# Optimization experiments

Measured on AMD Instinct MI355X. Metric: run time of the kernel, lower is better.

## Reference

```python
import jax, jax.numpy as jnp
import numpy as np

NUM_CLASSES = 7


def setup_inputs() -> dict:
    key = jax.random.key(0)
    k1, k2, k3, k4 = jax.random.split(key, 4)
    B, C, D = 65536, NUM_CLASSES, 512
    outputs = jax.random.normal(k1, (B, C), dtype=jnp.float32)
    features = jax.random.normal(k2, (B, D), dtype=jnp.float32)
    targets = jax.random.randint(k3, (B,), 0, C, dtype=jnp.int64)
    attention_weights = jax.random.uniform(k4, (B, D), dtype=jnp.float32)
    return {"outputs": outputs, "features": features, "targets": targets,
            "attention_weights": attention_weights}


def reference(outputs, features, targets, attention_weights):
    lambda_val = 0.1
    B = features.shape[0]
    C = outputs.shape[1]

    # Cross-entropy (mean over batch), matching nn.CrossEntropyLoss
    logp = jax.nn.log_softmax(outputs, axis=-1)  # [B, C]
    ce_loss = -jnp.mean(jnp.take_along_axis(logp, targets[:, None], axis=1))

    # Per-class centers via segment reduce (replaces python loop over classes)
    sums = jax.ops.segment_sum(features, targets, num_segments=C)      # [C, D]
    counts = jax.ops.segment_sum(jnp.ones((B,), features.dtype), targets,
                                 num_segments=C)                        # [C]
    present = counts > 0
    centers = sums / jnp.maximum(counts, 1.0)[:, None]                  # [C, D]

    # Squared distance to own-class center (replaces python loop over batch);
    # samples whose class is absent (impossible here, but kept faithful) add 0.
    diff = features - centers[targets]                                  # [B, D]
    per_sample = jnp.sum(diff * diff, axis=-1) * present[targets].astype(features.dtype)
    center_loss = jnp.sum(per_sample) / B

    l1_loss = jnp.mean(jnp.abs(attention_weights))

    total_loss = ce_loss + lambda_val * center_loss + 0.01 * l1_loss
    return (total_loss, ce_loss, center_loss, l1_loss)
```

## Files before the change

### kernel.cpp

```cpp
#include <hip/hip_runtime.h>

static constexpr int BATCH = 65536;
static constexpr int DDIM  = 512;
static constexpr int NCLS  = 7;
static constexpr int SLICE = NCLS * DDIM;
static constexpr int NSC   = 64;

struct WS {
  double sumsq_s[NSC];
  double l1_s[NSC];
  double ce_s[NSC];
  double wcss;
  double pad;
  float  counts_s[NSC][8];
};
static_assert(sizeof(WS) <= 4096, "header must fit in 4 KB");

__global__ __launch_bounds__(512, 6) void k_main(const float4* __restrict__ F,
                                                 const float4* __restrict__ A,
                                                 const int* __restrict__ tg,
                                                 const float* __restrict__ outputs,
                                                 float* __restrict__ part,
                                                 WS* __restrict__ ws,
                                                 int rpb) {
  const int tid  = threadIdx.x;
  const int bid  = blockIdx.x;
  const int c4   = tid & 127;
  const int ph   = tid >> 7;
  const int slot = bid & (NSC - 1);
  const int base = bid * rpb;

  float4 acc[NCLS];
#pragma unroll
  for (int c = 0; c < NCLS; ++c) acc[c] = make_float4(0.f, 0.f, 0.f, 0.f);
  float sumsq = 0.f, l1 = 0.f;

#pragma unroll 2
  for (int r = base; r < base + rpb; r += 8) {
    const int4 ta = *reinterpret_cast<const int4*>(tg + r);
    const int4 tb = *reinterpret_cast<const int4*>(tg + r + 4);
    const size_t i0 = (size_t)(r + ph) * 128 + c4;
    const float4 f0 = F[i0];
    const float4 f1 = F[i0 + 512];
    const float4 w0 = A[i0];
    const float4 w1 = A[i0 + 512];
    const int t0 = (ph == 0) ? ta.x : (ph == 1) ? ta.y : (ph == 2) ? ta.z : ta.w;
    const int t1 = (ph == 0) ? tb.x : (ph == 1) ? tb.y : (ph == 2) ? tb.z : tb.w;

    sumsq = fmaf(f0.x, f0.x, sumsq); sumsq = fmaf(f0.y, f0.y, sumsq);
    sumsq = fmaf(f0.z, f0.z, sumsq); sumsq = fmaf(f0.w, f0.w, sumsq);
    sumsq = fmaf(f1.x, f1.x, sumsq); sumsq = fmaf(f1.y, f1.y, sumsq);
    sumsq = fmaf(f1.z, f1.z, sumsq); sumsq = fmaf(f1.w, f1.w, sumsq);
    l1 += fabsf(w0.x) + fabsf(w0.y) + fabsf(w0.z) + fabsf(w0.w) +
          fabsf(w1.x) + fabsf(w1.y) + fabsf(w1.z) + fabsf(w1.w);

#pragma unroll
    for (int c = 0; c < NCLS; ++c) {
      acc[c].x += (t0 == c) ? f0.x : 0.f;
      acc[c].y += (t0 == c) ? f0.y : 0.f;
      acc[c].z += (t0 == c) ? f0.z : 0.f;
      acc[c].w += (t0 == c) ? f0.w : 0.f;
      acc[c].x += (t1 == c) ? f1.x : 0.f;
      acc[c].y += (t1 == c) ? f1.y : 0.f;
      acc[c].z += (t1 == c) ? f1.z : 0.f;
      acc[c].w += (t1 == c) ? f1.w : 0.f;
    }
  }

  __shared__ float red[256][33];
  if (ph >= 2) {
    float* row = red[(ph - 2) * 128 + c4];
#pragma unroll
    for (int c = 0; c < NCLS; ++c) {
      row[c * 4 + 0] = acc[c].x; row[c * 4 + 1] = acc[c].y;
      row[c * 4 + 2] = acc[c].z; row[c * 4 + 3] = acc[c].w;
    }
    row[28] = sumsq; row[29] = l1;
  }
  __syncthreads();
  if (ph < 2) {
    const float* row = red[ph * 128 + c4];
#pragma unroll
    for (int c = 0; c < NCLS; ++c) {
      acc[c].x += row[c * 4 + 0]; acc[c].y += row[c * 4 + 1];
      acc[c].z += row[c * 4 + 2]; acc[c].w += row[c * 4 + 3];
    }
    sumsq += row[28]; l1 += row[29];
  }
  __syncthreads();
  if (ph == 1) {
    float* row = red[c4];
#pragma unroll
    for (int c = 0; c < NCLS; ++c) {
      row[c * 4 + 0] = acc[c].x; row[c * 4 + 1] = acc[c].y;
      row[c * 4 + 2] = acc[c].z; row[c * 4 + 3] = acc[c].w;
    }
    row[28] = sumsq; row[29] = l1;
  }
  __syncthreads();

  __shared__ float s2[2], s3[2];
  if (ph == 0) {
    const float* row = red[c4];
#pragma unroll
    for (int c = 0; c < NCLS; ++c) {
      acc[c].x += row[c * 4 + 0]; acc[c].y += row[c * 4 + 1];
      acc[c].z += row[c * 4 + 2]; acc[c].w += row[c * 4 + 3];
    }
    sumsq += row[28]; l1 += row[29];

    float4* __restrict__ myp = reinterpret_cast<float4*>(part + (size_t)bid * SLICE);
#pragma unroll
    for (int c = 0; c < NCLS; ++c) myp[c * 128 + c4] = acc[c];

    float bs = sumsq, bl = l1;
#pragma unroll
    for (int off = 32; off > 0; off >>= 1) {
      bs += __shfl_down(bs, off);
      bl += __shfl_down(bl, off);
    }
    if ((tid & 63) == 0) { s2[tid >> 6] = bs; s3[tid >> 6] = bl; }
  }
  __syncthreads();
  if (tid == 0) {
    atomicAdd(&ws->sumsq_s[slot], (double)(s2[0] + s2[1]));
    atomicAdd(&ws->l1_s[slot],    (double)(s3[0] + s3[1]));
  }

  const int lane = tid & 63, wid = tid >> 6;
  if (wid * 64 < rpb) {
    float ce = 0.f;
    float cw[NCLS];
#pragma unroll
    for (int c = 0; c < NCLS; ++c) cw[c] = 0.f;
    for (int r0 = wid * 64; r0 < rpb; r0 += 512) {
      const int r = r0 + lane;
      const bool ok = (r < rpb);
      const int row = base + (ok ? r : 0);
      const float* o = outputs + (size_t)row * NCLS;
      const float x0 = o[0], x1 = o[1], x2 = o[2], x3 = o[3],
                  x4 = o[4], x5 = o[5], x6 = o[6];
      const float m = fmaxf(fmaxf(fmaxf(x0, x1), fmaxf(x2, x3)),
                            fmaxf(fmaxf(x4, x5), x6));
      const float s = expf(x0 - m) + expf(x1 - m) + expf(x2 - m) + expf(x3 - m) +
                      expf(x4 - m) + expf(x5 - m) + expf(x6 - m);
      const int t = ok ? tg[row] : -1;
      const float xt = (t == 0) ? x0 : (t == 1) ? x1 : (t == 2) ? x2 :
                       (t == 3) ? x3 : (t == 4) ? x4 : (t == 5) ? x5 : x6;
      ce += ok ? ((m - xt) + logf(s)) : 0.f;
#pragma unroll
      for (int c = 0; c < NCLS; ++c)
        cw[c] += (float)__popcll(__ballot(t == c)) * ((lane == 0) ? 1.f : 0.f);
    }
#pragma unroll
    for (int off = 32; off > 0; off >>= 1) ce += __shfl_down(ce, off);
    if (lane == 0) {
      atomicAdd(&ws->ce_s[slot], (double)ce);
#pragma unroll
      for (int c = 0; c < NCLS; ++c) atomicAdd(&ws->counts_s[slot][c], cw[c]);
    }
  }
}

__global__ __launch_bounds__(256) void k_reduce(const float* __restrict__ part,
                                                WS* __restrict__ ws, int nblk) {
  const int c  = blockIdx.x >> 4;
  const int cg = blockIdx.x & 15;
  const int t  = threadIdx.x;
  const int col = cg * 32 + (t & 31);
  const int sl0 = t >> 5;

  float s = 0.f;
#pragma unroll 4
  for (int sl = sl0; sl < nblk; sl += 8)
    s += part[(size_t)sl * SLICE + c * DDIM + col];

  __shared__ float red[8][33];
  red[sl0][t & 31] = s;

  __shared__ float scnt;
  if (t < 64) {
    float cv = ws->counts_s[t][c];
#pragma unroll
    for (int off = 32; off > 0; off >>= 1) cv += __shfl_down(cv, off);
    if (t == 0) scnt = cv;
  }
  __syncthreads();

  if (t < 32) {
    float S = 0.f;
#pragma unroll
    for (int i = 0; i < 8; ++i) S += red[i][t];
    float q = S * S;
#pragma unroll
    for (int off = 16; off > 0; off >>= 1) q += __shfl_down(q, off);
    if (t == 0 && scnt > 0.f) atomicAdd(&ws->wcss, (double)(q / scnt));
  }
}

__global__ __launch_bounds__(64) void k_fin(const WS* __restrict__ ws,
                                            float* __restrict__ out) {
  const int t = threadIdx.x;
  double a = ws->sumsq_s[t], b = ws->l1_s[t], d = ws->ce_s[t];
#pragma unroll
  for (int off = 32; off > 0; off >>= 1) {
    a += __shfl_down(a, off);
    b += __shfl_down(b, off);
    d += __shfl_down(d, off);
  }
  if (t == 0) {
    const double center = (a - ws->wcss) / (double)BATCH;
    const double ce = d / (double)BATCH;
    const double l1 = b / ((double)BATCH * (double)DDIM);
    out[0] = (float)(ce + 0.1 * center + 0.01 * l1);
    out[1] = (float)ce;
    out[2] = (float)center;
    out[3] = (float)l1;
  }
}

extern "C" void kernel_launch(void* const* d_in, const int* in_sizes, int n_in,
                              void* d_out, int out_size, void* d_ws, size_t ws_size,
                              hipStream_t stream) {
  const float*  outputs  = (const float*)d_in[0];
  const float4* features = (const float4*)d_in[1];
  const int*    targets  = (const int*)d_in[2];
  const float4* aw       = (const float4*)d_in[3];
  float* out = (float*)d_out;
  WS* ws = (WS*)d_ws;
  float* part = (float*)((char*)d_ws + 4096);

  const size_t avail = (ws_size > 4096) ? ws_size - 4096 : 0;
  int nblk = 128;
  if (avail >= (size_t)1024 * SLICE * 4) nblk = 1024;
  else if (avail >= (size_t)512 * SLICE * 4) nblk = 512;
  else if (avail >= (size_t)256 * SLICE * 4) nblk = 256;
  const int rpb = BATCH / nblk;

  hipMemsetAsync(d_ws, 0, 4096, stream);

  k_main<<<nblk, 512, 0, stream>>>(features, aw, targets, outputs, part, ws, rpb);
  k_reduce<<<NCLS * 16, 256, 0, stream>>>(part, ws, nblk);
  k_fin<<<1, 64, 0, stream>>>(ws, out);
}
```

Before: 70.75 us.

## Replace global atomics and memset with per-block scalar partials; template rows-per-block

Drops the workspace memset and the double-precision global atomics for sumsq, l1, ce and class counts. Each block now writes its scalar partials next to its per-class feature sums, and a wider final kernel reduces them. Rows-per-block becomes a template parameter so bounds checks vanish. The maximum grid is capped at 512 blocks instead of 1024, which may lower parallelism in the main streaming kernel.

```diff
diff --git a/kernel.cpp b/kernel.cpp
--- a/kernel.cpp
+++ b/kernel.cpp
@@ -1,34 +1,23 @@
 #include <hip/hip_runtime.h>
 
-static constexpr int BATCH = 65536;
-static constexpr int DDIM  = 512;
-static constexpr int NCLS  = 7;
-static constexpr int SLICE = NCLS * DDIM;
-static constexpr int NSC   = 64;
-
-struct WS {
-  double sumsq_s[NSC];
-  double l1_s[NSC];
-  double ce_s[NSC];
-  double wcss;
-  double pad;
-  float  counts_s[NSC][8];
-};
-static_assert(sizeof(WS) <= 4096, "header must fit in 4 KB");
-
+static constexpr int BATCH  = 65536;
+static constexpr int DDIM   = 512;
+static constexpr int NCLS   = 7;
+static constexpr int SLICE  = NCLS * DDIM;
+static constexpr int SLICEP = SLICE + 16;
+static constexpr int NRED   = NCLS * 16;
+
+template <int RPB>
 __global__ __launch_bounds__(512, 6) void k_main(const float4* __restrict__ F,
                                                  const float4* __restrict__ A,
                                                  const int* __restrict__ tg,
                                                  const float* __restrict__ outputs,
-                                                 float* __restrict__ part,
-                                                 WS* __restrict__ ws,
-                                                 int rpb) {
+                                                 float* __restrict__ part) {
   const int tid  = threadIdx.x;
   const int bid  = blockIdx.x;
   const int c4   = tid & 127;
   const int ph   = tid >> 7;
-  const int slot = bid & (NSC - 1);
-  const int base = bid * rpb;
+  const int base = bid * RPB;
 
   float4 acc[NCLS];
 #pragma unroll
@@ -36,7 +25,7 @@
   float sumsq = 0.f, l1 = 0.f;
 
 #pragma unroll 2
-  for (int r = base; r < base + rpb; r += 8) {
+  for (int r = base; r < base + RPB; r += 8) {
     const int4 ta = *reinterpret_cast<const int4*>(tg + r);
     const int4 tb = *reinterpret_cast<const int4*>(tg + r + 4);
     const size_t i0 = (size_t)(r + ph) * 128 + c4;
@@ -109,7 +98,7 @@
     }
     sumsq += row[28]; l1 += row[29];
 
-    float4* __restrict__ myp = reinterpret_cast<float4*>(part + (size_t)bid * SLICE);
+    float4* __restrict__ myp = reinterpret_cast<float4*>(part + (size_t)bid * SLICEP);
 #pragma unroll
     for (int c = 0; c < NCLS; ++c) myp[c * 128 + c4] = acc[c];
 
@@ -121,22 +110,18 @@
     }
     if ((tid & 63) == 0) { s2[tid >> 6] = bs; s3[tid >> 6] = bl; }
   }
-  __syncthreads();
-  if (tid == 0) {
-    atomicAdd(&ws->sumsq_s[slot], (double)(s2[0] + s2[1]));
-    atomicAdd(&ws->l1_s[slot],    (double)(s3[0] + s3[1]));
-  }
-
+
+  constexpr int NACT = (RPB / 64 < 8) ? RPB / 64 : 8;
+  __shared__ float ce_w[8];
+  __shared__ float cw_w[8][8];
   const int lane = tid & 63, wid = tid >> 6;
-  if (wid * 64 < rpb) {
+  if (wid < NACT) {
     float ce = 0.f;
     float cw[NCLS];
 #pragma unroll
     for (int c = 0; c < NCLS; ++c) cw[c] = 0.f;
-    for (int r0 = wid * 64; r0 < rpb; r0 += 512) {
-      const int r = r0 + lane;
-      const bool ok = (r < rpb);
-      const int row = base + (ok ? r : 0);
+    for (int r0 = wid * 64; r0 < RPB; r0 += NACT * 64) {
+      const int row = base + r0 + lane;
       const float* o = outputs + (size_t)row * NCLS;
       const float x0 = o[0], x1 = o[1], x2 = o[2], x3 = o[3],
                   x4 = o[4], x5 = o[5], x6 = o[6];
@@ -144,10 +129,10 @@
                             fmaxf(fmaxf(x4, x5), x6));
       const float s = expf(x0 - m) + expf(x1 - m) + expf(x2 - m) + expf(x3 - m) +
                       expf(x4 - m) + expf(x5 - m) + expf(x6 - m);
-      const int t = ok ? tg[row] : -1;
+      const int t = tg[row];
       const float xt = (t == 0) ? x0 : (t == 1) ? x1 : (t == 2) ? x2 :
                        (t == 3) ? x3 : (t == 4) ? x4 : (t == 5) ? x5 : x6;
-      ce += ok ? ((m - xt) + logf(s)) : 0.f;
+      ce += (m - xt) + logf(s);
 #pragma unroll
       for (int c = 0; c < NCLS; ++c)
         cw[c] += (float)__popcll(__ballot(t == c)) * ((lane == 0) ? 1.f : 0.f);
@@ -155,15 +140,35 @@
 #pragma unroll
     for (int off = 32; off > 0; off >>= 1) ce += __shfl_down(ce, off);
     if (lane == 0) {
-      atomicAdd(&ws->ce_s[slot], (double)ce);
-#pragma unroll
-      for (int c = 0; c < NCLS; ++c) atomicAdd(&ws->counts_s[slot][c], cw[c]);
-    }
+      ce_w[wid] = ce;
+#pragma unroll
+      for (int c = 0; c < NCLS; ++c) cw_w[wid][c] = cw[c];
+    }
+  }
+  __syncthreads();
+
+  if (tid == 0) {
+    float ceb = 0.f, cb[NCLS];
+#pragma unroll
+    for (int c = 0; c < NCLS; ++c) cb[c] = 0.f;
+#pragma unroll
+    for (int w = 0; w < NACT; ++w) {
+      ceb += ce_w[w];
+#pragma unroll
+      for (int c = 0; c < NCLS; ++c) cb[c] += cw_w[w][c];
+    }
+    float* sp = part + (size_t)bid * SLICEP + SLICE;
+    sp[0] = s2[0] + s2[1];
+    sp[1] = s3[0] + s3[1];
+    sp[2] = ceb;
+#pragma unroll
+    for (int c = 0; c < NCLS; ++c) sp[3 + c] = cb[c];
   }
 }
 
 __global__ __launch_bounds__(256) void k_reduce(const float* __restrict__ part,
-                                                WS* __restrict__ ws, int nblk) {
+                                                double* __restrict__ qpart,
+                                                int nblk) {
   const int c  = blockIdx.x >> 4;
   const int cg = blockIdx.x & 15;
   const int t  = threadIdx.x;
@@ -173,18 +178,10 @@
   float s = 0.f;
 #pragma unroll 4
   for (int sl = sl0; sl < nblk; sl += 8)
-    s += part[(size_t)sl * SLICE + c * DDIM + col];
+    s += part[(size_t)sl * SLICEP + c * DDIM + col];
 
   __shared__ float red[8][33];
   red[sl0][t & 31] = s;
-
-  __shared__ float scnt;
-  if (t < 64) {
-    float cv = ws->counts_s[t][c];
-#pragma unroll
-    for (int off = 32; off > 0; off >>= 1) cv += __shfl_down(cv, off);
-    if (t == 0) scnt = cv;
-  }
   __syncthreads();
 
   if (t < 32) {
@@ -194,28 +191,86 @@
     float q = S * S;
 #pragma unroll
     for (int off = 16; off > 0; off >>= 1) q += __shfl_down(q, off);
-    if (t == 0 && scnt > 0.f) atomicAdd(&ws->wcss, (double)(q / scnt));
+    if (t == 0) qpart[blockIdx.x] = (double)q;
   }
 }
 
-__global__ __launch_bounds__(64) void k_fin(const WS* __restrict__ ws,
-                                            float* __restrict__ out) {
+__global__ __launch_bounds__(512) void k_fin(const float* __restrict__ part,
+                                             const double* __restrict__ qpart,
+                                             float* __restrict__ out, int nblk) {
   const int t = threadIdx.x;
-  double a = ws->sumsq_s[t], b = ws->l1_s[t], d = ws->ce_s[t];
+  const int lane = t & 63, wid = t >> 6;
+
+  double ss = 0.0, l1 = 0.0, ce = 0.0;
+  float cnt[NCLS];
+#pragma unroll
+  for (int c = 0; c < NCLS; ++c) cnt[c] = 0.f;
+  for (int sl = t; sl < nblk; sl += 512) {
+    const float* sp = part + (size_t)sl * SLICEP + SLICE;
+    ss += (double)sp[0];
+    l1 += (double)sp[1];
+    ce += (double)sp[2];
+#pragma unroll
+    for (int c = 0; c < NCLS; ++c) cnt[c] += sp[3 + c];
+  }
+
 #pragma unroll
   for (int off = 32; off > 0; off >>= 1) {
-    a += __shfl_down(a, off);
-    b += __shfl_down(b, off);
-    d += __shfl_down(d, off);
-  }
+    ss += __shfl_down(ss, off);
+    l1 += __shfl_down(l1, off);
+    ce += __shfl_down(ce, off);
+#pragma unroll
+    for (int c = 0; c < NCLS; ++c) cnt[c] += __shfl_down(cnt[c], off);
+  }
+
+  __shared__ double lss[8], ll1[8], lce[8];
+  __shared__ float lcnt[8][8];
+  if (lane == 0) {
+    lss[wid] = ss; ll1[wid] = l1; lce[wid] = ce;
+#pragma unroll
+    for (int c = 0; c < NCLS; ++c) lcnt[wid][c] = cnt[c];
+  }
+  __syncthreads();
+
+  __shared__ float counts_sh[NCLS];
+  __shared__ double tot[3];
   if (t == 0) {
-    const double center = (a - ws->wcss) / (double)BATCH;
-    const double ce = d / (double)BATCH;
-    const double l1 = b / ((double)BATCH * (double)DDIM);
-    out[0] = (float)(ce + 0.1 * center + 0.01 * l1);
-    out[1] = (float)ce;
+    double a = 0, b = 0, d = 0;
+    float cc[NCLS];
+#pragma unroll
+    for (int c = 0; c < NCLS; ++c) cc[c] = 0.f;
+#pragma unroll
+    for (int w = 0; w < 8; ++w) {
+      a += lss[w]; b += ll1[w]; d += lce[w];
+#pragma unroll
+      for (int c = 0; c < NCLS; ++c) cc[c] += lcnt[w][c];
+    }
+    tot[0] = a; tot[1] = b; tot[2] = d;
+#pragma unroll
+    for (int c = 0; c < NCLS; ++c) counts_sh[c] = cc[c];
+  }
+  __syncthreads();
+
+  double myq = 0.0;
+  if (t < NRED) {
+    const float cn = counts_sh[t >> 4];
+    myq = (cn > 0.f) ? qpart[t] / (double)cn : 0.0;
+  }
+#pragma unroll
+  for (int off = 32; off > 0; off >>= 1) myq += __shfl_down(myq, off);
+  __shared__ double qs[2];
+  if (lane == 0 && wid < 2) qs[wid] = myq;
+  __syncthreads();
+
+  if (t == 0) {
+    const double wcss = qs[0] + qs[1];
+    const double center = (tot[0] - wcss) / (double)BATCH;
+    const double cem = tot[2] / (double)BATCH;
+    const double l1m = tot[1] / ((double)BATCH * (double)DDIM);
+    out[0] = (float)(cem + 0.1 * center + 0.01 * l1m);
+    out[1] = (float)cem;
     out[2] = (float)center;
-    out[3] = (float)l1;
+    out[3] = (float)l1m;
   }
 }
 
@@ -227,19 +282,19 @@
   const int*    targets  = (const int*)d_in[2];
   const float4* aw       = (const float4*)d_in[3];
   float* out = (float*)d_out;
-  WS* ws = (WS*)d_ws;
-  float* part = (float*)((char*)d_ws + 4096);
-
-  const size_t avail = (ws_size > 4096) ? ws_size - 4096 : 0;
+  float* part = (float*)d_ws;
+
+  auto need = [](int nblk) { return (size_t)nblk * SLICEP * 4 + NRED * 8; };
   int nblk = 128;
-  if (avail >= (size_t)1024 * SLICE * 4) nblk = 1024;
-  else if (avail >= (size_t)512 * SLICE * 4) nblk = 512;
-  else if (avail >= (size_t)256 * SLICE * 4) nblk = 256;
-  const int rpb = BATCH / nblk;
-
-  hipMemsetAsync(d_ws, 0, 4096, stream);
-
-  k_main<<<nblk, 512, 0, stream>>>(features, aw, targets, outputs, part, ws, rpb);
-  k_reduce<<<NCLS * 16, 256, 0, stream>>>(part, ws, nblk);
-  k_fin<<<1, 64, 0, stream>>>(ws, out);
+  if (ws_size >= need(512)) nblk = 512;
+  else if (ws_size >= need(256)) nblk = 256;
+  double* qpart = (double*)((char*)d_ws + (size_t)nblk * SLICEP * 4);
+
+  switch (nblk) {
+    case 512: k_main<128><<<512, 512, 0, stream>>>(features, aw, targets, outputs, part); break;
+    case 256: k_main<256><<<256, 512, 0, stream>>>(features, aw, targets, outputs, part); break;
+    default:  k_main<512><<<128, 512, 0, stream>>>(features, aw, targets, outputs, part); break;
+  }
+  k_reduce<<<NRED, 256, 0, stream>>>(part, qpart, nblk);
+  k_fin<<<1, 512, 0, stream>>>(part, qpart, out, nblk);
 }
```

After: 60.77 us. 1.16x faster.
